# Kernel optimization log

Measured on AMD Instinct MI355X. Metric: run time of the kernel, lower is better.

## Reference

```python
import jax, jax.numpy as jnp
import numpy as np

K = 10  # neighbor_num from init_kwargs


def setup_inputs() -> dict:
    key = jax.random.key(0)
    k1, k2 = jax.random.split(key)
    xyz = jax.random.normal(k1, (8, 16384, 3), dtype=jnp.float32)
    sample_xyz = jax.random.normal(k2, (8, 1024, 3), dtype=jnp.float32)
    temp = jnp.ones((), dtype=jnp.float32)  # init_temp = 1.0
    return {"xyz": xyz, "sample_xyz": sample_xyz, "temp": temp}


def reference(xyz, sample_xyz, temp):
    # Pairwise squared distances [B, S, N] via ||a-b||^2 = ||a||^2 + ||b||^2 - 2 a.b
    q2 = jnp.sum(sample_xyz * sample_xyz, axis=-1)            # [B, S]
    p2 = jnp.sum(xyz * xyz, axis=-1)                          # [B, N]
    cross = jnp.einsum('bsd,bnd->bsn', sample_xyz, xyz)       # [B, S, N]
    d2 = q2[:, :, None] + p2[:, None, :] - 2.0 * cross
    d2 = jnp.maximum(d2, 0.0)
    # K nearest neighbors (smallest squared distance)
    neg_top, idx = jax.lax.top_k(-d2, K)                      # [B, S, K]
    squared_dist = -neg_top
    # Gather neighbor coordinates: [B, S, K, 3]
    neighbor_xyz = jax.vmap(lambda pts, ids: pts[ids])(xyz, idx)
    # Softmax weights over the K neighbors
    weight = jax.nn.softmax(-squared_dist / (temp * temp), axis=-1)  # [B, S, K]
    proj_xyz = jnp.sum(neighbor_xyz * weight[..., None], axis=-2)    # [B, S, 3]
    return (proj_xyz, temp)
```

## Files before the change

kernel.cpp:

```cpp
#include <hip/hip_runtime.h>
#include <math.h>

#define NPTS 16384
#define NSMP 8192
#define KNN 10
#define QPB 8
#define WAVES 8
#define SLICE 2048
#define GPW 16
#define CAP 64
#define LCAP 160

typedef float v2f __attribute__((ext_vector_type(2)));
typedef unsigned long long u64;

__device__ __forceinline__ unsigned mapf(float f) {
    unsigned u = __float_as_uint(f);
    return (u & 0x80000000u) ? ~u : (u | 0x80000000u);
}
__device__ __forceinline__ float unmapf(unsigned k) {
    unsigned u = (k & 0x80000000u) ? (k ^ 0x80000000u) : ~k;
    return __uint_as_float(u);
}
__device__ __forceinline__ float uniform_f(float x) {
    return __uint_as_float(__builtin_amdgcn_readfirstlane(__float_as_uint(x)));
}

__global__ __launch_bounds__(256) void pack_kernel(const float* __restrict__ xyz,
                                                   float4* __restrict__ pk,
                                                   float4* __restrict__ pk2) {
    const int t = blockIdx.x * 256 + threadIdx.x;
    const int b = t >> 13;
    const int r = t & 8191;
    const int g = r >> 6;
    const int l = r & 63;
    const float* pA = xyz + ((size_t)b * NPTS + (size_t)g * 128 + l) * 3;
    const float* pB = pA + 64 * 3;
    const float xA = pA[0], yA = pA[1], zA = pA[2];
    const float xB = pB[0], yB = pB[1], zB = pB[2];
    const float wA = fmaf(xA, xA, fmaf(yA, yA, zA * zA));
    const float wB = fmaf(xB, xB, fmaf(yB, yB, zB * zB));
    float4* dst = pk + ((size_t)(b * 128 + g) * 128);
    dst[l]      = make_float4(xA, xB, yA, yB);
    dst[l + 64] = make_float4(zA, zB, wA, wB);
    float4* dst2 = pk2 + (size_t)b * NPTS + (size_t)g * 128;
    dst2[l]      = make_float4(xA, yA, zA, wA);
    dst2[l + 64] = make_float4(xB, yB, zB, wB);
}

__global__ __launch_bounds__(512) void knn_kernel(
    const float4* __restrict__ pk,
    const float4* __restrict__ pk2,
    const float* __restrict__ sxyz,
    const float* __restrict__ temp,
    float* __restrict__ out)
{
    __shared__ float minBuf[QPB][WAVES * 64];
    __shared__ int   cnt[QPB];
    __shared__ int   list[QPB][LCAP];
    __shared__ u64   candK[QPB][CAP];
    __shared__ u64   sort10[QPB][KNN];

    const int lane  = threadIdx.x & 63;
    const int w     = threadIdx.x >> 6;
    const int qbase = blockIdx.x * QPB;
    const int b     = qbase >> 10;

    if (threadIdx.x < QPB) cnt[threadIdx.x] = 0;

    float ax[QPB], ay[QPB], az[QPB];
    #pragma unroll
    for (int q = 0; q < QPB; ++q) {
        const float* s = sxyz + (size_t)(qbase + q) * 3;
        ax[q] = uniform_f(-2.f * s[0]);
        ay[q] = uniform_f(-2.f * s[1]);
        az[q] = uniform_f(-2.f * s[2]);
    }

    const float4* pw = pk + ((size_t)(b * 128 + w * 16)) * 128 + lane;

    v2f mn[QPB];
    #pragma unroll
    for (int q = 0; q < QPB; ++q) { mn[q].x = INFINITY; mn[q].y = INFINITY; }

    #pragma unroll 1
    for (int j = 0; j < GPW; j += 4) {
        const float4 a0 = pw[(size_t)(j + 0) * 128], a1 = pw[(size_t)(j + 0) * 128 + 64];
        const float4 b0 = pw[(size_t)(j + 1) * 128], b1 = pw[(size_t)(j + 1) * 128 + 64];
        const float4 e0 = pw[(size_t)(j + 2) * 128], e1 = pw[(size_t)(j + 2) * 128 + 64];
        const float4 f0 = pw[(size_t)(j + 3) * 128], f1 = pw[(size_t)(j + 3) * 128 + 64];
        {
            const v2f X = {a0.x, a0.y}, Y = {a0.z, a0.w}, Z = {a1.x, a1.y}, W = {a1.z, a1.w};
            #pragma unroll
            for (int q = 0; q < QPB; ++q) {
                const v2f d = X * ax[q] + (Y * ay[q] + (Z * az[q] + W));
                mn[q] = __builtin_elementwise_min(mn[q], d);
            }
        }
        {
            const v2f X = {b0.x, b0.y}, Y = {b0.z, b0.w}, Z = {b1.x, b1.y}, W = {b1.z, b1.w};
            #pragma unroll
            for (int q = 0; q < QPB; ++q) {
                const v2f d = X * ax[q] + (Y * ay[q] + (Z * az[q] + W));
                mn[q] = __builtin_elementwise_min(mn[q], d);
            }
        }
        {
            const v2f X = {e0.x, e0.y}, Y = {e0.z, e0.w}, Z = {e1.x, e1.y}, W = {e1.z, e1.w};
            #pragma unroll
            for (int q = 0; q < QPB; ++q) {
                const v2f d = X * ax[q] + (Y * ay[q] + (Z * az[q] + W));
                mn[q] = __builtin_elementwise_min(mn[q], d);
            }
        }
        {
            const v2f X = {f0.x, f0.y}, Y = {f0.z, f0.w}, Z = {f1.x, f1.y}, W = {f1.z, f1.w};
            #pragma unroll
            for (int q = 0; q < QPB; ++q) {
                const v2f d = X * ax[q] + (Y * ay[q] + (Z * az[q] + W));
                mn[q] = __builtin_elementwise_min(mn[q], d);
            }
        }
    }
    #pragma unroll
    for (int q = 0; q < QPB; ++q) minBuf[q][w * 64 + lane] = fminf(mn[q].x, mn[q].y);
    __syncthreads();

    const int gid = qbase + w;
    const float* sq = sxyz + (size_t)gid * 3;
    const float bx = -2.f * sq[0], by = -2.f * sq[1], bz = -2.f * sq[2];

    float mi[WAVES];
    #pragma unroll
    for (int k = 0; k < WAVES; ++k) mi[k] = minBuf[w][k * 64 + lane];
    float vm = mi[0];
    #pragma unroll
    for (int k = 1; k < WAVES; ++k) vm = fminf(vm, mi[k]);
    const unsigned um = mapf(vm);
    unsigned lo = 0u, hi = 0xFFFFFFFFu;
    #pragma unroll 1
    for (int it = 0; it < 16; ++it) {
        const unsigned mid = lo + ((hi - lo) >> 1);
        const int c = __popcll(__ballot(um <= mid));
        if (c >= KNN) hi = mid; else lo = mid + 1;
    }
    const float tau = unmapf(hi);

    int nf = 0;
    #pragma unroll
    for (int k = 0; k < WAVES; ++k) {
        const bool flg = (mi[k] <= tau);
        const u64 m = __ballot(flg);
        const int pos = nf + __popcll(m & ((1ull << lane) - 1ull));
        if (flg && pos < LCAP) list[w][pos] = k * 64 + lane;
        nf += __popcll(m);
    }
    if (nf > LCAP) nf = LCAP;

    const float4* p2 = pk2 + (size_t)b * NPTS;
    const int total = nf * 32;
    for (int i = lane; i < total; i += 64) {
        const int sid = list[w][i >> 5];
        const int p   = i & 31;
        const int idx = ((sid >> 6) << 11) + ((p >> 1) << 7) + ((p & 1) << 6) + (sid & 63);
        const float4 pt = p2[idx];
        const float d = fmaf(pt.x, bx, fmaf(pt.y, by, fmaf(pt.z, bz, pt.w)));
        if (d <= tau) {
            const int s = atomicAdd(&cnt[w], 1);
            if (s < CAP) candK[w][s] = ((u64)mapf(d) << 32) | (unsigned)idx;
        }
    }

    {
        const int c = min(cnt[w], CAP);
        const u64 k0 = (lane < c) ? candK[w][lane] : ~0ull;
        int r0 = 0;
        for (int jj = 0; jj < c; ++jj) {
            const u64 kj = candK[w][jj];
            r0 += (kj < k0) ? 1 : 0;
        }
        if (lane < c && r0 < KNN) sort10[w][r0] = k0;
        const u64 sel = (lane < KNN) ? sort10[w][lane] : ~0ull;

        const float q2 = fmaf(sq[0], sq[0], fmaf(sq[1], sq[1], sq[2] * sq[2]));
        const float dp = unmapf((unsigned)(sel >> 32));
        const float d2v = fmaxf(dp + q2, 0.f);
        const float dmin = __shfl(d2v, 0);
        const float t = temp[0];
        const float invt2 = 1.0f / (t * t);
        float wgt = 0.f, px = 0.f, py = 0.f, pz = 0.f;
        if (lane < KNN) {
            wgt = __expf((dmin - d2v) * invt2);
            const int idx = (int)(unsigned)(sel & 0xFFFFFFFFull);
            const float4 pp = p2[idx];
            px = pp.x; py = pp.y; pz = pp.z;
        }
        float sw = wgt, sx = wgt * px, sy = wgt * py, sz = wgt * pz;
        #pragma unroll
        for (int off = 8; off >= 1; off >>= 1) {
            sw += __shfl_xor(sw, off);
            sx += __shfl_xor(sx, off);
            sy += __shfl_xor(sy, off);
            sz += __shfl_xor(sz, off);
        }
        if (lane == 0) {
            const float inv = 1.0f / sw;
            out[(size_t)gid * 3 + 0] = sx * inv;
            out[(size_t)gid * 3 + 1] = sy * inv;
            out[(size_t)gid * 3 + 2] = sz * inv;
            if (gid == 0) out[NSMP * 3] = t;
        }
    }
}

extern "C" void kernel_launch(void* const* d_in, const int* in_sizes, int n_in,
                              void* d_out, int out_size, void* d_ws, size_t ws_size,
                              hipStream_t stream) {
    const float* xyz  = (const float*)d_in[0];
    const float* sxyz = (const float*)d_in[1];
    const float* temp = (const float*)d_in[2];
    float* out = (float*)d_out;

    float4* pk  = (float4*)d_ws;
    float4* pk2 = (float4*)((char*)d_ws + (size_t)131072*16);

    hipLaunchKernelGGL(pack_kernel, dim3(256), dim3(256), 0, stream, xyz, pk, pk2);
    hipLaunchKernelGGL(knn_kernel, dim3(NSMP / QPB), dim3(512), 0, stream,
                       pk, pk2, sxyz, temp, out);
}
```

Baseline: 41.46 us.

## Halve waves per block, keep per-lane pair minima, each wave handles two queries

The KNN block shrinks from 8 to 4 waves, so each wave scans 32 point-groups instead of 16. Per-lane minima are now kept separately for the two point halves instead of being merged, which gives finer 64-point slices with 32 points each to rescan. Each wave then runs the threshold and selection phase for two queries in sequence. The intent is to cut per-block overhead and make the candidate rescan more selective, at the cost of a longer scan per wave and a serialised selection phase.

```diff
diff --git a/kernel.cpp b/kernel.cpp
--- a/kernel.cpp
+++ b/kernel.cpp
@@ -5,11 +5,11 @@
 #define NSMP 8192
 #define KNN 10
 #define QPB 8
-#define WAVES 8
-#define SLICE 2048
-#define GPW 16
+#define WAVES 4
+#define SLICE 4096
+#define GPW 32
 #define CAP 64
-#define LCAP 160
+#define LCAP 128
 
 typedef float v2f __attribute__((ext_vector_type(2)));
 typedef unsigned long long u64;
@@ -48,16 +48,16 @@
     dst2[l + 64] = make_float4(xB, yB, zB, wB);
 }
 
-__global__ __launch_bounds__(512) void knn_kernel(
+__global__ __launch_bounds__(256) void knn_kernel(
     const float4* __restrict__ pk,
     const float4* __restrict__ pk2,
     const float* __restrict__ sxyz,
     const float* __restrict__ temp,
     float* __restrict__ out)
 {
-    __shared__ float minBuf[QPB][WAVES * 64];
+    __shared__ float minBuf[QPB][512];
     __shared__ int   cnt[QPB];
-    __shared__ int   list[QPB][LCAP];
+    __shared__ int   list[WAVES][LCAP];
     __shared__ u64   candK[QPB][CAP];
     __shared__ u64   sort10[QPB][KNN];
 
@@ -77,18 +77,16 @@
         az[q] = uniform_f(-2.f * s[2]);
     }
 
-    const float4* pw = pk + ((size_t)(b * 128 + w * 16)) * 128 + lane;
+    const float4* pw = pk + ((size_t)(b * 128 + w * 32)) * 128 + lane;
 
     v2f mn[QPB];
     #pragma unroll
     for (int q = 0; q < QPB; ++q) { mn[q].x = INFINITY; mn[q].y = INFINITY; }
 
     #pragma unroll 1
-    for (int j = 0; j < GPW; j += 4) {
+    for (int j = 0; j < GPW; j += 2) {
         const float4 a0 = pw[(size_t)(j + 0) * 128], a1 = pw[(size_t)(j + 0) * 128 + 64];
         const float4 b0 = pw[(size_t)(j + 1) * 128], b1 = pw[(size_t)(j + 1) * 128 + 64];
-        const float4 e0 = pw[(size_t)(j + 2) * 128], e1 = pw[(size_t)(j + 2) * 128 + 64];
-        const float4 f0 = pw[(size_t)(j + 3) * 128], f1 = pw[(size_t)(j + 3) * 128 + 64];
         {
             const v2f X = {a0.x, a0.y}, Y = {a0.z, a0.w}, Z = {a1.x, a1.y}, W = {a1.z, a1.w};
             #pragma unroll
@@ -105,89 +103,80 @@
                 mn[q] = __builtin_elementwise_min(mn[q], d);
             }
         }
-        {
-            const v2f X = {e0.x, e0.y}, Y = {e0.z, e0.w}, Z = {e1.x, e1.y}, W = {e1.z, e1.w};
-            #pragma unroll
-            for (int q = 0; q < QPB; ++q) {
-                const v2f d = X * ax[q] + (Y * ay[q] + (Z * az[q] + W));
-                mn[q] = __builtin_elementwise_min(mn[q], d);
+    }
+    #pragma unroll
+    for (int q = 0; q < QPB; ++q) {
+        minBuf[q][w * 128 + lane]      = mn[q].x;
+        minBuf[q][w * 128 + 64 + lane] = mn[q].y;
+    }
+    __syncthreads();
+
+    const float4* p2 = pk2 + (size_t)b * NPTS;
+    const float t = temp[0];
+    const float invt2 = 1.0f / (t * t);
+
+    #pragma unroll 1
+    for (int qi = 0; qi < 2; ++qi) {
+        const int rq  = w + qi * WAVES;
+        const int gid = qbase + rq;
+        const float* sq = sxyz + (size_t)gid * 3;
+        const float bx = -2.f * sq[0], by = -2.f * sq[1], bz = -2.f * sq[2];
+
+        float mh[8];
+        #pragma unroll
+        for (int s8 = 0; s8 < 8; ++s8)
+            mh[s8] = minBuf[rq][(s8 >> 1) * 128 + (s8 & 1) * 64 + lane];
+
+        float vm = mh[0];
+        #pragma unroll
+        for (int s8 = 1; s8 < 8; ++s8) vm = fminf(vm, mh[s8]);
+        const unsigned um = mapf(vm);
+        unsigned lo = 0u, hi = 0xFFFFFFFFu;
+        #pragma unroll 1
+        for (int it = 0; it < 16; ++it) {
+            const unsigned mid = lo + ((hi - lo) >> 1);
+            const int c = __popcll(__ballot(um <= mid));
+            if (c >= KNN) hi = mid; else lo = mid + 1;
+        }
+        const float tau = unmapf(hi);
+
+        int nf = 0;
+        #pragma unroll
+        for (int s8 = 0; s8 < 8; ++s8) {
+            const bool flg = (mh[s8] <= tau);
+            const u64 m = __ballot(flg);
+            const int pos = nf + __popcll(m & ((1ull << lane) - 1ull));
+            if (flg && pos < LCAP) list[w][pos] = (s8 >> 1) * 128 + (s8 & 1) * 64 + lane;
+            nf += __popcll(m);
+        }
+        if (nf > LCAP) nf = LCAP;
+
+        const int total = nf * 32;
+        for (int i = lane; i < total; i += 64) {
+            const int s   = list[w][i >> 5];
+            const int idx = ((s >> 7) << 12) + ((i & 31) << 7) + (s & 127);
+            const float4 pt = p2[idx];
+            const float d = fmaf(pt.x, bx, fmaf(pt.y, by, fmaf(pt.z, bz, pt.w)));
+            if (d <= tau) {
+                const int sl = atomicAdd(&cnt[rq], 1);
+                if (sl < CAP) candK[rq][sl] = ((u64)mapf(d) << 32) | (unsigned)idx;
             }
         }
-        {
-            const v2f X = {f0.x, f0.y}, Y = {f0.z, f0.w}, Z = {f1.x, f1.y}, W = {f1.z, f1.w};
-            #pragma unroll
-            for (int q = 0; q < QPB; ++q) {
-                const v2f d = X * ax[q] + (Y * ay[q] + (Z * az[q] + W));
-                mn[q] = __builtin_elementwise_min(mn[q], d);
-            }
-        }
-    }
-    #pragma unroll
-    for (int q = 0; q < QPB; ++q) minBuf[q][w * 64 + lane] = fminf(mn[q].x, mn[q].y);
-    __syncthreads();
-
-    const int gid = qbase + w;
-    const float* sq = sxyz + (size_t)gid * 3;
-    const float bx = -2.f * sq[0], by = -2.f * sq[1], bz = -2.f * sq[2];
-
-    float mi[WAVES];
-    #pragma unroll
-    for (int k = 0; k < WAVES; ++k) mi[k] = minBuf[w][k * 64 + lane];
-    float vm = mi[0];
-    #pragma unroll
-    for (int k = 1; k < WAVES; ++k) vm = fminf(vm, mi[k]);
-    const unsigned um = mapf(vm);
-    unsigned lo = 0u, hi = 0xFFFFFFFFu;
-    #pragma unroll 1
-    for (int it = 0; it < 16; ++it) {
-        const unsigned mid = lo + ((hi - lo) >> 1);
-        const int c = __popcll(__ballot(um <= mid));
-        if (c >= KNN) hi = mid; else lo = mid + 1;
-    }
-    const float tau = unmapf(hi);
-
-    int nf = 0;
-    #pragma unroll
-    for (int k = 0; k < WAVES; ++k) {
-        const bool flg = (mi[k] <= tau);
-        const u64 m = __ballot(flg);
-        const int pos = nf + __popcll(m & ((1ull << lane) - 1ull));
-        if (flg && pos < LCAP) list[w][pos] = k * 64 + lane;
-        nf += __popcll(m);
-    }
-    if (nf > LCAP) nf = LCAP;
-
-    const float4* p2 = pk2 + (size_t)b * NPTS;
-    const int total = nf * 32;
-    for (int i = lane; i < total; i += 64) {
-        const int sid = list[w][i >> 5];
-        const int p   = i & 31;
-        const int idx = ((sid >> 6) << 11) + ((p >> 1) << 7) + ((p & 1) << 6) + (sid & 63);
-        const float4 pt = p2[idx];
-        const float d = fmaf(pt.x, bx, fmaf(pt.y, by, fmaf(pt.z, bz, pt.w)));
-        if (d <= tau) {
-            const int s = atomicAdd(&cnt[w], 1);
-            if (s < CAP) candK[w][s] = ((u64)mapf(d) << 32) | (unsigned)idx;
-        }
-    }
-
-    {
-        const int c = min(cnt[w], CAP);
-        const u64 k0 = (lane < c) ? candK[w][lane] : ~0ull;
+
+        const int c = min(cnt[rq], CAP);
+        const u64 k0 = (lane < c) ? candK[rq][lane] : ~0ull;
         int r0 = 0;
         for (int jj = 0; jj < c; ++jj) {
-            const u64 kj = candK[w][jj];
+            const u64 kj = candK[rq][jj];
             r0 += (kj < k0) ? 1 : 0;
         }
-        if (lane < c && r0 < KNN) sort10[w][r0] = k0;
-        const u64 sel = (lane < KNN) ? sort10[w][lane] : ~0ull;
+        if (lane < c && r0 < KNN) sort10[rq][r0] = k0;
+        const u64 sel = (lane < KNN) ? sort10[rq][lane] : ~0ull;
 
         const float q2 = fmaf(sq[0], sq[0], fmaf(sq[1], sq[1], sq[2] * sq[2]));
         const float dp = unmapf((unsigned)(sel >> 32));
         const float d2v = fmaxf(dp + q2, 0.f);
         const float dmin = __shfl(d2v, 0);
-        const float t = temp[0];
-        const float invt2 = 1.0f / (t * t);
         float wgt = 0.f, px = 0.f, py = 0.f, pz = 0.f;
         if (lane < KNN) {
             wgt = __expf((dmin - d2v) * invt2);
@@ -225,6 +214,6 @@
     float4* pk2 = (float4*)((char*)d_ws + (size_t)131072*16);
 
     hipLaunchKernelGGL(pack_kernel, dim3(256), dim3(256), 0, stream, xyz, pk, pk2);
-    hipLaunchKernelGGL(knn_kernel, dim3(NSMP / QPB), dim3(512), 0, stream,
+    hipLaunchKernelGGL(knn_kernel, dim3(NSMP / QPB), dim3(256), 0, stream,
                        pk, pk2, sxyz, temp, out);
 }
```

Measured after the change: 40.08 us, median of 2. 3.3% less time.
